# Performance work log

Hardware: AMD Instinct MI355X
Metric: run time of the kernel (lower is better)

Reference implementation:

```python
import jax, jax.numpy as jnp
import numpy as np

MEM, KEY, VAL, DIN, BS, BQ = 1000, 64, 128, 512, 512, 65536


def setup_inputs() -> dict:
    key = jax.random.key(0)
    ks = jax.random.split(key, 20)

    def lin(k, fan_in, shape):
        return (jax.random.normal(k, shape, jnp.float32) / np.sqrt(fan_in)).astype(jnp.float32)

    return {
        "support_x": jax.random.normal(ks[0], (BS, DIN), jnp.float32),
        "support_y": jax.random.normal(ks[1], (BS, VAL), jnp.float32),
        "query_x": jax.random.normal(ks[2], (BQ, DIN), jnp.float32),
        "query_y": jax.random.normal(ks[3], (BQ, 1), jnp.float32),
        # base model: Linear(DIN -> KEY)
        "base_W": lin(ks[4], DIN, (DIN, KEY)),
        "base_b": jnp.zeros((KEY,), jnp.float32),
        # ExternalMemory projections
        "kp_W": lin(ks[5], KEY, (KEY, KEY)),
        "kp_b": jnp.zeros((KEY,), jnp.float32),
        "vp_W": lin(ks[6], VAL, (VAL, VAL)),
        "vp_b": jnp.zeros((VAL,), jnp.float32),
        # memory buffers (randn keys/values like register_buffer(torch.randn))
        "mem_keys": jax.random.normal(ks[7], (MEM, KEY), jnp.float32),
        "mem_values": jax.random.normal(ks[8], (MEM, VAL), jnp.float32),
        # ages: uniform so top-k picks distinct slots deterministically
        "mem_age": jax.random.uniform(ks[9], (MEM,), jnp.float32),
        # controller MLP: Linear(KEY+VAL,128) ReLU Linear(128,64) ReLU Linear(64,1)
        "c1_W": lin(ks[10], KEY + VAL, (KEY + VAL, 128)),
        "c1_b": jnp.zeros((128,), jnp.float32),
        "c2_W": lin(ks[11], 128, (128, 64)),
        "c2_b": jnp.zeros((64,), jnp.float32),
        "c3_W": lin(ks[12], 64, (64, 1)),
        "c3_b": jnp.zeros((1,), jnp.float32),
    }


def reference(support_x, support_y, query_x, query_y,
              base_W, base_b, kp_W, kp_b, vp_W, vp_b,
              mem_keys, mem_values, mem_age,
              c1_W, c1_b, c2_W, c2_b, c3_W, c3_b):
    # base model features
    support_feat = support_x @ base_W + base_b          # [BS, KEY]
    query_feat = query_x @ base_W + base_b              # [BQ, KEY]

    # --- memory.write(support_feat, support_y) ---
    proj_keys = support_feat @ kp_W + kp_b              # [BS, KEY]
    proj_vals = support_y @ vp_W + vp_b                 # [BS, VAL]
    _, oldest = jax.lax.top_k(mem_age, BS)              # evict oldest BS slots
    new_keys = mem_keys.at[oldest].set(proj_keys)       # [MEM, KEY]
    new_values = mem_values.at[oldest].set(proj_vals)   # [MEM, VAL]

    # --- memory.read(query_feat) ---
    proj_q = query_feat @ kp_W + kp_b                   # [BQ, KEY]
    sims = proj_q @ new_keys.T                          # [BQ, MEM]
    attn = jax.nn.softmax(sims, axis=-1)
    retrieved = attn @ new_values                       # [BQ, VAL]

    # --- controller MLP on [query_feat ; retrieved] ---
    aug = jnp.concatenate([query_feat, retrieved], axis=-1)  # [BQ, KEY+VAL]
    h = jax.nn.relu(aug @ c1_W + c1_b)
    h = jax.nn.relu(h @ c2_W + c2_b)
    query_pred = h @ c3_W + c3_b                        # [BQ, 1]

    meta_loss = jnp.mean((query_pred - query_y) ** 2)
    return meta_loss, query_pred, retrieved
```

## Files before the change

kernel.cpp:

```cpp
#include <hip/hip_runtime.h>

typedef _Float16 h8v __attribute__((ext_vector_type(8)));
typedef _Float16 h4v __attribute__((ext_vector_type(4)));
typedef float    f4v __attribute__((ext_vector_type(4)));

#define MFMA16(a,b,c) __builtin_amdgcn_mfma_f32_16x16x32_f16((a),(b),(c),0,0,0)
#define NEGF (-1e30f)

#define MEM 1000
#define KEY 64
#define VAL 128
#define DIN 512
#define BS  512
#define BQ  65536


typedef __attribute__((address_space(1))) const unsigned int guint;
typedef __attribute__((address_space(3))) unsigned int luint;

__device__ __forceinline__ void gld16(const _Float16* g, _Float16* l)
{
  __builtin_amdgcn_global_load_lds((guint*)g, (luint*)l, 16, 0, 0);
}

__device__ __forceinline__ h8v cvt8(const float* p)
{
  f4v u = *(const f4v*)p;
  f4v v = *(const f4v*)(p + 4);
  h8v a;
  a[0] = (_Float16)u.x; a[1] = (_Float16)u.y; a[2] = (_Float16)u.z; a[3] = (_Float16)u.w;
  a[4] = (_Float16)v.x; a[5] = (_Float16)v.y; a[6] = (_Float16)v.z; a[7] = (_Float16)v.w;
  return a;
}

__device__ __forceinline__ h8v cvt8nt(const float* p)
{
  f4v u = __builtin_nontemporal_load((const f4v*)p);
  f4v v = __builtin_nontemporal_load((const f4v*)(p + 4));
  h8v a;
  a[0] = (_Float16)u.x; a[1] = (_Float16)u.y; a[2] = (_Float16)u.z; a[3] = (_Float16)u.w;
  a[4] = (_Float16)v.x; a[5] = (_Float16)v.y; a[6] = (_Float16)v.z; a[7] = (_Float16)v.w;
  return a;
}

__global__ void k_prep1(const float* __restrict__ baseW, const float* __restrict__ base_b,
                        const float* __restrict__ kpW, const float* __restrict__ kp_b,
                        const float* __restrict__ vpW, const float* __restrict__ c1W,
                        const float* __restrict__ c2W, const float* __restrict__ age,
                        _Float16* __restrict__ WTf, float* __restrict__ bcomb,
                        _Float16* __restrict__ vpWt, _Float16* __restrict__ c1F,
                        _Float16* __restrict__ c2F, int* __restrict__ ranks,
                        float* __restrict__ out0)
{
  long id = (long)blockIdx.x * 256 + threadIdx.x;
  if (id < 65536) {
    int h = (int)id;
    int j = h & 7, lane = (h >> 3) & 63, KS = (h >> 9) & 15, F = h >> 13;
    int n = F * 16 + (lane & 15);
    int k = KS * 32 + ((lane >> 4) << 3) + j;
    float v;
    if (n < 64) v = baseW[(size_t)k * 64 + n];
    else {
      int nn = n - 64;
      const float* br = baseW + (size_t)k * 64;
      float s = 0.f;
      for (int t = 0; t < 64; ++t) s += br[t] * kpW[t * 64 + nn];
      v = s;
    }
    WTf[h] = (_Float16)v;
  } else if (id < 65664) {
    int i = (int)(id - 65536);
    if (i < 64) bcomb[i] = base_b[i];
    else {
      int n = i - 64;
      float s = kp_b[n];
      for (int t = 0; t < 64; ++t) s += base_b[t] * kpW[t * 64 + n];
      bcomb[i] = s;
    }
  } else if (id < 90240) {
    int h = (int)(id - 65664);
    int j = h & 7, lane = (h >> 3) & 63, KS = (h >> 9) % 6, F = (h >> 9) / 6;
    int n = F * 16 + (lane & 15);
    int k = KS * 32 + ((lane >> 4) << 3) + j;
    c1F[h] = (_Float16)c1W[(size_t)k * 128 + n];
  } else if (id < 98432) {
    int h = (int)(id - 90240);
    int j = h & 7, lane = (h >> 3) & 63, KS = (h >> 9) & 3, F = h >> 11;
    int n = F * 16 + (lane & 15);
    int k = KS * 32 + ((lane >> 4) << 3) + j;
    c2F[h] = (_Float16)c2W[(size_t)k * 64 + n];
  } else if (id < 114816) {
    long i = id - 98432;
    int n = (int)(i >> 7), k = (int)(i & 127);
    vpWt[i] = (_Float16)vpW[(size_t)k * 128 + n];
  } else if (id < 115816) {
    int jx = (int)(id - 114816);
    float aj = age[jx];
    int r = 0;
    for (int i2 = 0; i2 < MEM; ++i2) {
      float ai = age[i2];
      r += (ai > aj) || (ai == aj && i2 < jx);
    }
    ranks[jx] = r;
  } else if (id == 115816) {
    *out0 = 0.f;
  }
}

__global__ __launch_bounds__(64) void k_prep2(
    const float* __restrict__ sx, const float* __restrict__ sy,
    const _Float16* __restrict__ WTf, const float* __restrict__ bcomb,
    const _Float16* __restrict__ vpWt, const float* __restrict__ vp_b,
    float* __restrict__ pkeys, float* __restrict__ pvals)
{
  const int lane = threadIdx.x, quad = lane >> 4, l15 = lane & 15;
  const f4v fz = {0.f, 0.f, 0.f, 0.f};
  if (blockIdx.x < 32) {
    const int m0 = blockIdx.x * 16;
    f4v acc[4];
    #pragma unroll
    for (int f = 0; f < 4; ++f) acc[f] = fz;
    const float* xr = sx + (size_t)(m0 + l15) * DIN;
    #pragma unroll 4
    for (int ks = 0; ks < 16; ++ks) {
      int k0 = ks * 32 + quad * 8;
      h8v a = cvt8(xr + k0);
      #pragma unroll
      for (int f = 0; f < 4; ++f) {
        h8v b = *(const h8v*)(WTf + (size_t)((((4 + f) * 16) + ks) * 64 + lane) * 8);
        acc[f] = MFMA16(a, b, acc[f]);
      }
    }
    #pragma unroll
    for (int f = 0; f < 4; ++f) {
      int col = f * 16 + l15;
      float bb = bcomb[64 + col];
      #pragma unroll
      for (int r = 0; r < 4; ++r)
        pkeys[(size_t)(m0 + quad * 4 + r) * KEY + col] = acc[f][r] + bb;
    }
  } else {
    const int m0 = (blockIdx.x - 32) * 16;
    f4v acc[8];
    #pragma unroll
    for (int f = 0; f < 8; ++f) acc[f] = fz;
    const float* yr = sy + (size_t)(m0 + l15) * VAL;
    #pragma unroll
    for (int ks = 0; ks < 4; ++ks) {
      int k0 = ks * 32 + quad * 8;
      h8v a = cvt8(yr + k0);
      #pragma unroll
      for (int f = 0; f < 8; ++f) {
        h8v b = *(const h8v*)(vpWt + (size_t)(f * 16 + l15) * 128 + k0);
        acc[f] = MFMA16(a, b, acc[f]);
      }
    }
    #pragma unroll
    for (int f = 0; f < 8; ++f) {
      int col = f * 16 + l15;
      float bb = vp_b[col];
      #pragma unroll
      for (int r = 0; r < 4; ++r)
        pvals[(size_t)(m0 + quad * 4 + r) * VAL + col] = acc[f][r] + bb;
    }
  }
}

__global__ void k_prep3(const int* __restrict__ ranks, const float* __restrict__ pk,
                        const float* __restrict__ pv, const float* __restrict__ memK,
                        const float* __restrict__ memV,
                        _Float16* __restrict__ keysF, _Float16* __restrict__ valF)
{
  int id = blockIdx.x * 256 + threadIdx.x;
  if (id < 65536) {
    int j = id & 7, lane = (id >> 3) & 63, KS = (id >> 9) & 1, F = id >> 10;
    int n = F * 16 + (lane & 15);
    int k = KS * 32 + ((lane >> 4) << 3) + j;
    float v = 0.f;
    if (n < MEM) {
      int rk = ranks[n];
      v = (rk < BS) ? pk[(size_t)rk * KEY + k] : memK[(size_t)n * KEY + k];
    }
    keysF[id] = (_Float16)v;
  } else {
    int h = id - 65536;
    int j = h & 7, lane = (h >> 3) & 63, KS = (h >> 9) & 31, F = h >> 14;
    int nv = F * 16 + (lane & 15);
    int jm = KS * 32 + ((j >> 2) << 4) + (((lane >> 4)) << 2) + (j & 3);
    float v = 0.f;
    if (jm < MEM) {
      int rk = ranks[jm];
      v = (rk < BS) ? pv[(size_t)rk * VAL + nv] : memV[(size_t)jm * VAL + nv];
    }
    valF[h] = (_Float16)v;
  }
}

__global__ __launch_bounds__(512, 4) void k_fused(
    const float* __restrict__ qx, const float* __restrict__ qy,
    const _Float16* __restrict__ WTf, const float* __restrict__ bcomb,
    const float* __restrict__ c1_b, const float* __restrict__ c2_b,
    const float* __restrict__ c3W, const float* __restrict__ c3b,
    const _Float16* __restrict__ c1F, const _Float16* __restrict__ c2F,
    const _Float16* __restrict__ keysF, const _Float16* __restrict__ valF,
    float* __restrict__ dout)
{
  __shared__ __align__(16) char smem[65536];
  _Float16* const Wq0 = (_Float16*)smem;
  _Float16* const Wq1 = (_Float16*)(smem + 32768);
  _Float16* const K0 = (_Float16*)smem;
  _Float16* const K1 = (_Float16*)(smem + 8192);
  _Float16* const V0 = (_Float16*)(smem + 16384);
  _Float16* const V1 = (_Float16*)(smem + 32768);

  const int tid  = threadIdx.x;
  const int wid  = tid >> 6;
  const int lane = tid & 63;
  const int quad = lane >> 4;
  const int l15  = lane & 15;

  _Float16* const qstash = (_Float16*)(smem + 49152 + wid * 2048);
  _Float16* const P_s  = (_Float16*)(smem + wid * 6656);
  _Float16* const h2_s = P_s + 2176;

  const int tile = blockIdx.x * 8 + wid;
  const int q0   = tile * 16;

  float* out_pred = dout + 1;
  float* out_ret  = dout + 1 + BQ;
  const f4v fz = {0.f, 0.f, 0.f, 0.f};

  #pragma unroll
  for (int i = 0; i < 4; ++i) {
    const int t = wid * 4 + i;
    const int f = t >> 2, ksq = t & 3;
    gld16(WTf + (size_t)(f * 16 + ksq) * 512 + lane * 8, Wq0 + t * 512);
  }
  asm volatile("s_waitcnt vmcnt(0)" ::: "memory");
  __syncthreads();

  f4v acc[8];
  #pragma unroll
  for (int f = 0; f < 8; ++f) acc[f] = fz;
  const float* xr = qx + (size_t)(q0 + l15) * DIN;

  #pragma unroll
  for (int q = 0; q < 4; ++q) {
    _Float16* const Wb = (q & 1) ? Wq1 : Wq0;
    _Float16* const Wn = (q & 1) ? Wq0 : Wq1;
    if (q < 3) {
      #pragma unroll
      for (int i = 0; i < 4; ++i) {
        const int t = wid * 4 + i;
        const int f = t >> 2, ksq = t & 3;
        gld16(WTf + (size_t)(f * 16 + (q + 1) * 4 + ksq) * 512 + lane * 8,
              Wn + t * 512);
      }
    }
    #pragma unroll
    for (int ksq = 0; ksq < 4; ++ksq) {
      const int ks = q * 4 + ksq;
      h8v a = cvt8nt(xr + ks * 32 + quad * 8);
      #pragma unroll
      for (int f = 0; f < 8; ++f) {
        h8v b = *(const h8v*)(Wb + (size_t)((f * 4 + ksq) * 64 + lane) * 8);
        acc[f] = MFMA16(a, b, acc[f]);
      }
    }
    asm volatile("s_waitcnt vmcnt(0)" ::: "memory");
    __syncthreads();
  }

  _Float16* tbuf = (_Float16*)(smem + wid * 4352);
  h8v pq0, pq1;
  {
    #pragma unroll
    for (int f = 0; f < 8; ++f) {
      float bb = bcomb[f * 16 + l15];
      #pragma unroll
      for (int r = 0; r < 4; ++r)
        tbuf[(quad * 4 + r) * 136 + f * 16 + l15] = (_Float16)(acc[f][r] + bb);
    }
    h8v qf0 = *(const h8v*)&tbuf[l15 * 136 +  0 + quad * 8];
    h8v qf1 = *(const h8v*)&tbuf[l15 * 136 + 32 + quad * 8];
    pq0 = *(const h8v*)&tbuf[l15 * 136 + 64 + quad * 8];
    pq1 = *(const h8v*)&tbuf[l15 * 136 + 96 + quad * 8];
    *(h8v*)&qstash[0 * 512 + lane * 8] = qf0;
    *(h8v*)&qstash[1 * 512 + lane * 8] = qf1;
  }
  __syncthreads();

  #pragma unroll
  for (int i = 0; i < 3; ++i) {
    const int t = wid * 3 + i;
    if (t < 8) gld16(keysF + (size_t)t * 512 + lane * 8, K0 + t * 512);
    else {
      const int tv = t - 8;
      gld16(valF + (size_t)((tv >> 1) * 32 + (tv & 1)) * 512 + lane * 8,
            V0 + tv * 512);
    }
  }
  asm volatile("s_waitcnt vmcnt(0)" ::: "memory");
  __syncthreads();

  float rm = NEGF, rl = 0.f;
  f4v O[8];
  #pragma unroll
  for (int v = 0; v < 8; ++v) O[v] = fz;

  #pragma unroll 1
  for (int c = 0; c < 16; ++c) {
    const int cur = c & 1;
    _Float16* const Kc = cur ? K1 : K0;
    _Float16* const Vc = cur ? V1 : V0;
    _Float16* const Kn = cur ? K0 : K1;
    _Float16* const Vn = cur ? V0 : V1;

    if (c < 15) {
      const int nc = c + 1;
      #pragma unroll
      for (int i = 0; i < 3; ++i) {
        const int t = wid * 3 + i;
        if (t < 8)
          gld16(keysF + (size_t)(nc * 8 + t) * 512 + lane * 8, Kn + t * 512);
        else {
          const int tv = t - 8;
          gld16(valF + (size_t)((tv >> 1) * 32 + nc * 2 + (tv & 1)) * 512 + lane * 8,
                Vn + tv * 512);
        }
      }
    }

    f4v S[4];
    #pragma unroll
    for (int f = 0; f < 4; ++f) S[f] = fz;
    #pragma unroll
    for (int f = 0; f < 4; ++f) {
      h8v b0 = *(const h8v*)(Kc + (size_t)(f * 2 + 0) * 512 + lane * 8);
      h8v b1 = *(const h8v*)(Kc + (size_t)(f * 2 + 1) * 512 + lane * 8);
      S[f] = MFMA16(b0, pq0, S[f]);
      S[f] = MFMA16(b1, pq1, S[f]);
    }

    float cm = NEGF;
    #pragma unroll
    for (int f = 0; f < 4; ++f) {
      const int sb = c * 64 + f * 16 + quad * 4;
      #pragma unroll
      for (int r = 0; r < 4; ++r) {
        float s = (sb + r < MEM) ? S[f][r] : NEGF;
        S[f][r] = s;
        cm = fmaxf(cm, s);
      }
    }
    cm = fmaxf(cm, __shfl_xor(cm, 16));
    cm = fmaxf(cm, __shfl_xor(cm, 32));
    float mn = fmaxf(rm, cm);
    float al = __expf(rm - mn);
    rm = mn;
    float psl = 0.f;
    #pragma unroll
    for (int f = 0; f < 4; ++f)
      #pragma unroll
      for (int r = 0; r < 4; ++r) {
        float p = __expf(S[f][r] - mn);
        S[f][r] = p;
        psl += p;
      }
    rl = rl * al + psl;
    float alO[4];
    #pragma unroll
    for (int r = 0; r < 4; ++r) alO[r] = __shfl(al, quad * 4 + r);
    #pragma unroll
    for (int v = 0; v < 8; ++v)
      #pragma unroll
      for (int r = 0; r < 4; ++r) O[v][r] *= alO[r];

    #pragma unroll
    for (int ks2 = 0; ks2 < 2; ++ks2) {
      h8v a;
      #pragma unroll
      for (int e = 0; e < 4; ++e) {
        a[e]     = (_Float16)S[2 * ks2][e];
        a[e + 4] = (_Float16)S[2 * ks2 + 1][e];
      }
      #pragma unroll
      for (int v = 0; v < 8; ++v) {
        h8v b = *(const h8v*)(Vc + (size_t)(v * 2 + ks2) * 512 + lane * 8);
        O[v] = MFMA16(a, b, O[v]);
      }
    }

    asm volatile("s_waitcnt vmcnt(0)" ::: "memory");
    __syncthreads();
  }

  rl += __shfl_xor(rl, 16); rl += __shfl_xor(rl, 32);
  float rlO[4];
  #pragma unroll
  for (int r = 0; r < 4; ++r) rlO[r] = __shfl(rl, quad * 4 + r);

  h8v qf0 = *(const h8v*)&qstash[0 * 512 + lane * 8];
  h8v qf1 = *(const h8v*)&qstash[1 * 512 + lane * 8];
  __syncthreads();

  #pragma unroll
  for (int v = 0; v < 8; ++v)
    #pragma unroll
    for (int r = 0; r < 4; ++r)
      P_s[(quad * 4 + r) * 136 + v * 16 + l15] = (_Float16)(O[v][r] / rlO[r]);

  #pragma unroll
  for (int it = 0; it < 8; ++it) {
    int flat = it * 256 + lane * 4;
    int row = flat >> 7, col = flat & 127;
    h4v t = *(const h4v*)&P_s[row * 136 + col];
    f4v o;
    o.x = (float)t[0]; o.y = (float)t[1]; o.z = (float)t[2]; o.w = (float)t[3];
    __builtin_nontemporal_store(o, (f4v*)(out_ret + (size_t)q0 * VAL + flat));
  }

  {
    f4v H[8];
    #pragma unroll
    for (int f = 0; f < 8; ++f) H[f] = fz;
    #pragma unroll
    for (int ks = 0; ks < 6; ++ks) {
      const int k0 = ks * 32;
      h8v a = (ks == 0) ? qf0 : (ks == 1) ? qf1
               : *(const h8v*)&P_s[l15 * 136 + (k0 - 64) + quad * 8];
      #pragma unroll
      for (int f = 0; f < 8; ++f) {
        h8v b = *(const h8v*)(c1F + (size_t)(f * 6 + ks) * 512 + lane * 8);
        H[f] = MFMA16(a, b, H[f]);
      }
    }
    #pragma unroll
    for (int f = 0; f < 8; ++f) {
      float bb = c1_b[f * 16 + l15];
      #pragma unroll
      for (int r = 0; r < 4; ++r)
        P_s[(quad * 4 + r) * 136 + f * 16 + l15] =
            (_Float16)fmaxf(0.f, H[f][r] + bb);
    }
  }

  {
    f4v G[4];
    #pragma unroll
    for (int f = 0; f < 4; ++f) G[f] = fz;
    #pragma unroll
    for (int ks = 0; ks < 4; ++ks) {
      h8v a = *(const h8v*)&P_s[l15 * 136 + ks * 32 + quad * 8];
      #pragma unroll
      for (int f = 0; f < 4; ++f) {
        h8v b = *(const h8v*)(c2F + (size_t)(f * 4 + ks) * 512 + lane * 8);
        G[f] = MFMA16(a, b, G[f]);
      }
    }
    #pragma unroll
    for (int f = 0; f < 4; ++f) {
      float bb = c2_b[f * 16 + l15];
      #pragma unroll
      for (int r = 0; r < 4; ++r)
        h2_s[(quad * 4 + r) * 72 + f * 16 + l15] =
            (_Float16)fmaxf(0.f, G[f][r] + bb);
    }
  }

  float lsum;
  {
    const int prow = lane >> 2, pj = lane & 3;
    float s = 0.f;
    #pragma unroll
    for (int k = 0; k < 16; ++k) {
      int kk = pj * 16 + k;
      s += (float)h2_s[prow * 72 + kk] * c3W[kk];
    }
    s += __shfl_xor(s, 1);
    s += __shfl_xor(s, 2);
    float pred = s + c3b[0];
    float diff = pred - qy[q0 + prow];
    if (pj == 0) out_pred[q0 + prow] = pred;
    lsum = diff * diff;
  }
  #pragma unroll
  for (int m = 1; m < 64; m <<= 1) lsum += __shfl_xor(lsum, m);
  if (lane == 0) atomicAdd(dout, lsum * (1.0f / (4.0f * (float)BQ)));
}

extern "C" void kernel_launch(void* const* d_in, const int* in_sizes, int n_in,
                              void* d_out, int out_size, void* d_ws, size_t ws_size,
                              hipStream_t stream)
{
  const float* support_x = (const float*)d_in[0];
  const float* support_y = (const float*)d_in[1];
  const float* query_x   = (const float*)d_in[2];
  const float* query_y   = (const float*)d_in[3];
  const float* base_W    = (const float*)d_in[4];
  const float* base_b    = (const float*)d_in[5];
  const float* kp_W      = (const float*)d_in[6];
  const float* kp_b      = (const float*)d_in[7];
  const float* vp_W      = (const float*)d_in[8];
  const float* vp_b      = (const float*)d_in[9];
  const float* mem_keys  = (const float*)d_in[10];
  const float* mem_vals  = (const float*)d_in[11];
  const float* mem_age   = (const float*)d_in[12];
  const float* c1_W      = (const float*)d_in[13];
  const float* c1_b      = (const float*)d_in[14];
  const float* c2_W      = (const float*)d_in[15];
  const float* c2_b      = (const float*)d_in[16];
  const float* c3_W      = (const float*)d_in[17];
  const float* c3_b      = (const float*)d_in[18];

  char* w = (char*)d_ws;
  _Float16* WTf   = (_Float16*)(w + 0);
  _Float16* vpWt  = (_Float16*)(w + 131072);
  _Float16* c1F   = (_Float16*)(w + 163840);
  _Float16* c2F   = (_Float16*)(w + 212992);
  float*    bcomb = (float*)   (w + 229376);
  int*      ranks = (int*)     (w + 229888);
  float*    pkeys = (float*)   (w + 233984);
  float*    pvals = (float*)   (w + 365056);
  _Float16* keysF = (_Float16*)(w + 627200);
  _Float16* valF  = (_Float16*)(w + 758272);

  float* out = (float*)d_out;

  hipLaunchKernelGGL(k_prep1, dim3(453), dim3(256), 0, stream,
                     base_W, base_b, kp_W, kp_b, vp_W, c1_W, c2_W, mem_age,
                     WTf, bcomb, vpWt, c1F, c2F, ranks, out);
  hipLaunchKernelGGL(k_prep2, dim3(64), dim3(64), 0, stream,
                     support_x, support_y, WTf, bcomb, vpWt, vp_b, pkeys, pvals);
  hipLaunchKernelGGL(k_prep3, dim3(768), dim3(256), 0, stream,
                     ranks, pkeys, pvals, mem_keys, mem_vals, keysF, valF);
  hipLaunchKernelGGL(k_fused, dim3(BQ / 128), dim3(512), 0, stream,
                     query_x, query_y, WTf, bcomb, c1_b, c2_b, c3_W, c3_b,
                     c1F, c2F, keysF, valF, out);
}
```

Baseline: 370.3 us.

## Replicate shared weights per block group and rotate chunk order to spread memory traffic

```diff
diff --git a/kernel.cpp b/kernel.cpp
--- a/kernel.cpp
+++ b/kernel.cpp
@@ -13,6 +13,7 @@
 #define DIN 512
 #define BS  512
 #define BQ  65536
+#define NCOPY 8
 
 
 typedef __attribute__((address_space(1))) const unsigned int guint;
@@ -169,11 +170,15 @@
 __global__ void k_prep3(const int* __restrict__ ranks, const float* __restrict__ pk,
                         const float* __restrict__ pv, const float* __restrict__ memK,
                         const float* __restrict__ memV,
-                        _Float16* __restrict__ keysF, _Float16* __restrict__ valF)
-{
-  int id = blockIdx.x * 256 + threadIdx.x;
-  if (id < 65536) {
-    int j = id & 7, lane = (id >> 3) & 63, KS = (id >> 9) & 1, F = id >> 10;
+                        _Float16* __restrict__ keysF, _Float16* __restrict__ valF,
+                        _Float16* __restrict__ WTf, _Float16* __restrict__ c1F,
+                        _Float16* __restrict__ c2F)
+{
+  long id = (long)blockIdx.x * 256 + threadIdx.x;
+  if (id < 8L * 65536) {
+    int h = (int)(id & 65535);
+    int copy = (int)(id >> 16);
+    int j = h & 7, lane = (h >> 3) & 63, KS = (h >> 9) & 1, F = h >> 10;
     int n = F * 16 + (lane & 15);
     int k = KS * 32 + ((lane >> 4) << 3) + j;
     float v = 0.f;
@@ -181,28 +186,42 @@
       int rk = ranks[n];
       v = (rk < BS) ? pk[(size_t)rk * KEY + k] : memK[(size_t)n * KEY + k];
     }
-    keysF[id] = (_Float16)v;
-  } else {
-    int h = id - 65536;
+    keysF[(size_t)copy * 65536 + h] = (_Float16)v;
+  } else if (id < 8L * 65536 + 8L * 131072) {
+    long i = id - 8L * 65536;
+    int h = (int)(i & 131071);
+    int copy = (int)(i >> 17);
     int j = h & 7, lane = (h >> 3) & 63, KS = (h >> 9) & 31, F = h >> 14;
     int nv = F * 16 + (lane & 15);
-    int jm = KS * 32 + ((j >> 2) << 4) + (((lane >> 4)) << 2) + (j & 3);
+    int jm = KS * 32 + ((j >> 2) << 4) + ((lane >> 4) << 2) + (j & 3);
     float v = 0.f;
     if (jm < MEM) {
       int rk = ranks[jm];
       v = (rk < BS) ? pv[(size_t)rk * VAL + nv] : memV[(size_t)jm * VAL + nv];
     }
-    valF[h] = (_Float16)v;
+    valF[(size_t)copy * 131072 + h] = (_Float16)v;
+  } else {
+    long i = id - (8L * 65536 + 8L * 131072);
+    if (i < 7L * 65536) {
+      int copy = 1 + (int)(i >> 16); int h = (int)(i & 65535);
+      WTf[(size_t)copy * 65536 + h] = WTf[h];
+    } else if ((i -= 7L * 65536) < 7L * 24576) {
+      int copy = 1 + (int)(i / 24576); int h = (int)(i % 24576);
+      c1F[(size_t)copy * 24576 + h] = c1F[h];
+    } else if ((i -= 7L * 24576) < 7L * 8192) {
+      int copy = 1 + (int)(i >> 13); int h = (int)(i & 8191);
+      c2F[(size_t)copy * 8192 + h] = c2F[h];
+    }
   }
 }
 
 __global__ __launch_bounds__(512, 4) void k_fused(
     const float* __restrict__ qx, const float* __restrict__ qy,
-    const _Float16* __restrict__ WTf, const float* __restrict__ bcomb,
+    const _Float16* __restrict__ WTf_, const float* __restrict__ bcomb,
     const float* __restrict__ c1_b, const float* __restrict__ c2_b,
     const float* __restrict__ c3W, const float* __restrict__ c3b,
-    const _Float16* __restrict__ c1F, const _Float16* __restrict__ c2F,
-    const _Float16* __restrict__ keysF, const _Float16* __restrict__ valF,
+    const _Float16* __restrict__ c1F_, const _Float16* __restrict__ c2F_,
+    const _Float16* __restrict__ keysF_, const _Float16* __restrict__ valF_,
     float* __restrict__ dout)
 {
   __shared__ __align__(16) char smem[65536];
@@ -219,6 +238,15 @@
   const int quad = lane >> 4;
   const int l15  = lane & 15;
 
+  const int cpy  = blockIdx.x & 7;
+  const int rot  = (blockIdx.x >> 3) & 15;
+  const int qrot = (blockIdx.x >> 1) & 3;
+  const _Float16* const WTf   = WTf_   + (size_t)cpy * 65536;
+  const _Float16* const c1F   = c1F_   + (size_t)cpy * 24576;
+  const _Float16* const c2F   = c2F_   + (size_t)cpy * 8192;
+  const _Float16* const keysF = keysF_ + (size_t)cpy * 65536;
+  const _Float16* const valF  = valF_  + (size_t)cpy * 131072;
+
   _Float16* const qstash = (_Float16*)(smem + 49152 + wid * 2048);
   _Float16* const P_s  = (_Float16*)(smem + wid * 6656);
   _Float16* const h2_s = P_s + 2176;
@@ -234,7 +262,7 @@
   for (int i = 0; i < 4; ++i) {
     const int t = wid * 4 + i;
     const int f = t >> 2, ksq = t & 3;
-    gld16(WTf + (size_t)(f * 16 + ksq) * 512 + lane * 8, Wq0 + t * 512);
+    gld16(WTf + (size_t)(f * 16 + qrot * 4 + ksq) * 512 + lane * 8, Wq0 + t * 512);
   }
   asm volatile("s_waitcnt vmcnt(0)" ::: "memory");
   __syncthreads();
@@ -246,20 +274,22 @@
 
   #pragma unroll
   for (int q = 0; q < 4; ++q) {
+    const int qe = (q + qrot) & 3;
     _Float16* const Wb = (q & 1) ? Wq1 : Wq0;
     _Float16* const Wn = (q & 1) ? Wq0 : Wq1;
     if (q < 3) {
+      const int qn = (q + 1 + qrot) & 3;
       #pragma unroll
       for (int i = 0; i < 4; ++i) {
         const int t = wid * 4 + i;
         const int f = t >> 2, ksq = t & 3;
-        gld16(WTf + (size_t)(f * 16 + (q + 1) * 4 + ksq) * 512 + lane * 8,
+        gld16(WTf + (size_t)(f * 16 + qn * 4 + ksq) * 512 + lane * 8,
               Wn + t * 512);
       }
     }
     #pragma unroll
     for (int ksq = 0; ksq < 4; ++ksq) {
-      const int ks = q * 4 + ksq;
+      const int ks = qe * 4 + ksq;
       h8v a = cvt8nt(xr + ks * 32 + quad * 8);
       #pragma unroll
       for (int f = 0; f < 8; ++f) {
@@ -293,10 +323,10 @@
   #pragma unroll
   for (int i = 0; i < 3; ++i) {
     const int t = wid * 3 + i;
-    if (t < 8) gld16(keysF + (size_t)t * 512 + lane * 8, K0 + t * 512);
+    if (t < 8) gld16(keysF + (size_t)(rot * 8 + t) * 512 + lane * 8, K0 + t * 512);
     else {
       const int tv = t - 8;
-      gld16(valF + (size_t)((tv >> 1) * 32 + (tv & 1)) * 512 + lane * 8,
+      gld16(valF + (size_t)((tv >> 1) * 32 + rot * 2 + (tv & 1)) * 512 + lane * 8,
             V0 + tv * 512);
     }
   }
@@ -310,6 +340,7 @@
 
   #pragma unroll 1
   for (int c = 0; c < 16; ++c) {
+    const int ce  = (c + rot) & 15;
     const int cur = c & 1;
     _Float16* const Kc = cur ? K1 : K0;
     _Float16* const Vc = cur ? V1 : V0;
@@ -317,15 +348,15 @@
     _Float16* const Vn = cur ? V0 : V1;
 
     if (c < 15) {
-      const int nc = c + 1;
+      const int ne = (c + 1 + rot) & 15;
       #pragma unroll
       for (int i = 0; i < 3; ++i) {
         const int t = wid * 3 + i;
         if (t < 8)
-          gld16(keysF + (size_t)(nc * 8 + t) * 512 + lane * 8, Kn + t * 512);
+          gld16(keysF + (size_t)(ne * 8 + t) * 512 + lane * 8, Kn + t * 512);
         else {
           const int tv = t - 8;
-          gld16(valF + (size_t)((tv >> 1) * 32 + nc * 2 + (tv & 1)) * 512 + lane * 8,
+          gld16(valF + (size_t)((tv >> 1) * 32 + ne * 2 + (tv & 1)) * 512 + lane * 8,
                 Vn + tv * 512);
         }
       }
@@ -345,7 +376,7 @@
     float cm = NEGF;
     #pragma unroll
     for (int f = 0; f < 4; ++f) {
-      const int sb = c * 64 + f * 16 + quad * 4;
+      const int sb = ce * 64 + f * 16 + quad * 4;
       #pragma unroll
       for (int r = 0; r < 4; ++r) {
         float s = (sb + r < MEM) ? S[f][r] : NEGF;
@@ -355,26 +386,29 @@
     }
     cm = fmaxf(cm, __shfl_xor(cm, 16));
     cm = fmaxf(cm, __shfl_xor(cm, 32));
-    float mn = fmaxf(rm, cm);
-    float al = __expf(rm - mn);
-    rm = mn;
+    if (__any(cm > rm)) {
+      float mn = fmaxf(rm, cm);
+      float al = __expf(rm - mn);
+      rm = mn;
+      float alO[4];
+      #pragma unroll
+      for (int r = 0; r < 4; ++r) alO[r] = __shfl(al, quad * 4 + r);
+      #pragma unroll
+      for (int v = 0; v < 8; ++v)
+        #pragma unroll
+        for (int r = 0; r < 4; ++r) O[v][r] *= alO[r];
+      rl *= al;
+    }
     float psl = 0.f;
     #pragma unroll
     for (int f = 0; f < 4; ++f)
       #pragma unroll
       for (int r = 0; r < 4; ++r) {
-        float p = __expf(S[f][r] - mn);
+        float p = __expf(S[f][r] - rm);
         S[f][r] = p;
         psl += p;
       }
-    rl = rl * al + psl;
-    float alO[4];
-    #pragma unroll
-    for (int r = 0; r < 4; ++r) alO[r] = __shfl(al, quad * 4 + r);
-    #pragma unroll
-    for (int v = 0; v < 8; ++v)
-      #pragma unroll
-      for (int r = 0; r < 4; ++r) O[v][r] *= alO[r];
+    rl += psl;
 
     #pragma unroll
     for (int ks2 = 0; ks2 < 2; ++ks2) {
@@ -515,15 +549,15 @@
 
   char* w = (char*)d_ws;
   _Float16* WTf   = (_Float16*)(w + 0);
-  _Float16* vpWt  = (_Float16*)(w + 131072);
-  _Float16* c1F   = (_Float16*)(w + 163840);
-  _Float16* c2F   = (_Float16*)(w + 212992);
-  float*    bcomb = (float*)   (w + 229376);
-  int*      ranks = (int*)     (w + 229888);
-  float*    pkeys = (float*)   (w + 233984);
-  float*    pvals = (float*)   (w + 365056);
-  _Float16* keysF = (_Float16*)(w + 627200);
-  _Float16* valF  = (_Float16*)(w + 758272);
+  _Float16* c1F   = (_Float16*)(w + 1048576);
+  _Float16* c2F   = (_Float16*)(w + 1441792);
+  _Float16* keysF = (_Float16*)(w + 1572864);
+  _Float16* valF  = (_Float16*)(w + 2621440);
+  _Float16* vpWt  = (_Float16*)(w + 4718592);
+  float*    bcomb = (float*)   (w + 4751360);
+  int*      ranks = (int*)     (w + 4751872);
+  float*    pkeys = (float*)   (w + 4755968);
+  float*    pvals = (float*)   (w + 4887040);
 
   float* out = (float*)d_out;
 
@@ -532,8 +566,9 @@
                      WTf, bcomb, vpWt, c1F, c2F, ranks, out);
   hipLaunchKernelGGL(k_prep2, dim3(64), dim3(64), 0, stream,
                      support_x, support_y, WTf, bcomb, vpWt, vp_b, pkeys, pvals);
-  hipLaunchKernelGGL(k_prep3, dim3(768), dim3(256), 0, stream,
-                     ranks, pkeys, pvals, mem_keys, mem_vals, keysF, valF);
+  hipLaunchKernelGGL(k_prep3, dim3(8832), dim3(256), 0, stream,
+                     ranks, pkeys, pvals, mem_keys, mem_vals, keysF, valF,
+                     WTf, c1F, c2F);
   hipLaunchKernelGGL(k_fused, dim3(BQ / 128), dim3(512), 0, stream,
                      query_x, query_y, WTf, bcomb, c1_b, c2_b, c3_W, c3_b,
                      c1F, c2F, keysF, valF, out);
```

Result: no change. 364.4 us (-1.6%).
